# Kernel optimization log

Measured on AMD Instinct MI355X. Metric: run time of the kernel, lower is better.

Reference implementation:

```python
import jax, jax.numpy as jnp
import numpy as np

B, T, H, D = 1, 2048, 32, 128
Q_GROUP = 4
HKV = H // Q_GROUP
INNER = H * D
KV_INNER = HKV * D
ROPE_BASE = 10000.0
NEG = -1e30


def _rope_tables(seq_len, head_dim, dtype):
    inv_freq = 1.0 / (ROPE_BASE ** (jnp.arange(0, head_dim, 2, dtype=jnp.float32) / head_dim))
    t = jnp.arange(seq_len, dtype=jnp.float32)
    freqs = jnp.einsum('t,f->tf', t, inv_freq)          # [T, D/2]
    emb = jnp.concatenate([freqs, freqs], axis=-1)      # [T, D]
    cos = jnp.cos(emb)[None, :, None, :].astype(dtype)  # [1, T, 1, D]
    sin = jnp.sin(emb)[None, :, None, :].astype(dtype)
    return cos, sin


def _rotate(x, cos, sin):
    # x: [B, T, H, D]; split-half rotation: cat(-x2, x1)
    half = x.shape[-1] // 2
    x1, x2 = x[..., :half], x[..., half:]
    x_rot = jnp.concatenate([-x2, x1], axis=-1)
    return x * cos + x_rot * sin


def setup_inputs() -> dict:
    key = jax.random.key(0)
    ks = jax.random.split(key, 5)
    return {
        'stm': jax.random.normal(ks[0], (B, T, H, D), dtype=jnp.float32),
        'w_q': jax.random.normal(ks[1], (INNER, INNER), dtype=jnp.float32) * 0.02,
        'w_k': jax.random.normal(ks[2], (KV_INNER, INNER), dtype=jnp.float32) * 0.02,
        'w_v': jax.random.normal(ks[3], (KV_INNER, INNER), dtype=jnp.float32) * 0.02,
        'w_o': jax.random.normal(ks[4], (INNER, INNER), dtype=jnp.float32) * 0.02,
    }


def reference(stm, w_q, w_k, w_v, w_o):
    b, t, h, d = stm.shape
    x = stm.reshape(b * t, h * d)
    q = x @ w_q.T                                   # [B*T, H*D]
    k = x @ w_k.T                                   # [B*T, Hkv*D]
    v = x @ w_v.T
    # GQA repeat_interleave over query-group axis (broadcast then reshape)
    k = jnp.broadcast_to(k.reshape(b * t, HKV, 1, d), (b * t, HKV, Q_GROUP, d)).reshape(b, t, h, d)
    v = jnp.broadcast_to(v.reshape(b * t, HKV, 1, d), (b * t, HKV, Q_GROUP, d)).reshape(b, t, h, d)
    q = q.reshape(b, t, h, d)
    cos, sin = _rope_tables(t, d, stm.dtype)        # prefill: seq_start = 0
    q = _rotate(q, cos, sin)
    k = _rotate(k, cos, sin)                        # rotated k is what gets written to the KV cache
    scale = 1.0 / np.sqrt(d)
    scores = jnp.einsum('bqhd,bkhd->bhqk', q, k).astype(jnp.float32) * scale
    causal = jnp.tril(jnp.ones((t, t), dtype=jnp.float32))          # mask_w
    bias = (1.0 - causal) * NEG                                     # mask_b
    scores = scores * causal[None, None] + bias[None, None]
    attn = jax.nn.softmax(scores, axis=-1).astype(stm.dtype)
    o = jnp.einsum('bhqk,bkhd->bqhd', attn, v)
    o = o.reshape(b * t, h * d) @ w_o.T
    return o.reshape(b, t, h, d)
```

## Files before the change

### kernel.cpp

```cpp
#include <hip/hip_runtime.h>
#include <hip/hip_bf16.h>
#include <stdint.h>
#include <stddef.h>

using bf16  = __hip_bfloat16;
using v4s   = __attribute__((ext_vector_type(4))) short;
using v8s   = __attribute__((ext_vector_type(8))) short;
using f32x4 = __attribute__((ext_vector_type(4))) float;

#define MFMA_16x16x32(a, b, c) __builtin_amdgcn_mfma_f32_16x16x32_bf16((a), (b), (c), 0, 0, 0)

__device__ __forceinline__ void async_lds16(const bf16* g, bf16* l) {
  __builtin_amdgcn_global_load_lds(
      (const __attribute__((address_space(1))) void*)g,
      (__attribute__((address_space(3))) void*)l, 16, 0, 0);
}

__device__ __forceinline__ short bf16_bits(float f) {
  bf16 h = __float2bfloat16(f);
  short s;
  __builtin_memcpy(&s, &h, sizeof(s));
  return s;
}

__global__ void cvt_f32_bf16(const float* __restrict__ in, bf16* __restrict__ out,
                             int n4) {
  const int i = blockIdx.x * blockDim.x + threadIdx.x;
  if (i >= n4) return;
  const float4 f = ((const float4*)in)[i];
  v4s o;
  o[0] = bf16_bits(f.x);
  o[1] = bf16_bits(f.y);
  o[2] = bf16_bits(f.z);
  o[3] = bf16_bits(f.w);
  *(v4s*)(out + (size_t)i * 4) = o;
}

template <bool F32OUT>
__global__ __launch_bounds__(512, 2) void gemm_bt8(const bf16* __restrict__ A,
                                                   const bf16* __restrict__ B,
                                                   void* __restrict__ C,
                                                   int M, int N, int K) {
  __shared__ bf16 lds[2][64][512];
  const int tid  = threadIdx.x;
  const int w    = tid >> 6;
  const int lane = tid & 63;
  const int quad = lane >> 4;
  const int m16  = lane & 15;
  const int wr = w >> 2, wc = w & 3;
  const int tm = blockIdx.y, tn = blockIdx.x;
  const int NKT = K >> 6;

  const bf16* Ast0 = A + (size_t)(tm * 256 + w * 16 + m16) * K + quad * 8;
  const bf16* Ast1 = Ast0 + (size_t)128 * K;
  const bf16* Bst0 = B + (size_t)(tn * 256 + w * 16 + m16) * K + quad * 8;
  const bf16* Bst1 = Bst0 + (size_t)128 * K;

  auto stage = [&](const bf16* g, bf16* l) {
    async_lds16(g, l);
    async_lds16(g + 32, l + 512);
  };

  f32x4 acc[8][4] = {};

  {
    bf16* L0 = &lds[0][0][0];
    bf16* L1 = &lds[1][0][0];
    stage(Bst0, L0 + (32 + w * 2) * 512);
    stage(Bst1, L0 + (48 + w * 2) * 512);
    stage(Ast0, L0 + (w * 2) * 512);
    stage(Ast1, L0 + (16 + w * 2) * 512);
    stage(Bst0 + 64, L1 + (32 + w * 2) * 512);
    stage(Bst1 + 64, L1 + (48 + w * 2) * 512);
    stage(Ast0 + 64, L1 + (w * 2) * 512);
  }
  asm volatile("s_waitcnt vmcnt(6)" ::: "memory");
  __builtin_amdgcn_s_barrier();

  for (int k = 0; k < NKT; ++k) {
    bf16* Lc = &lds[k & 1][0][0];
    bf16* Ln = &lds[(k & 1) ^ 1][0][0];
    v8s af[4][2], bfv[4][2];
#pragma unroll
    for (int mi = 0; mi < 4; ++mi) {
      af[mi][0] = *(const v8s*)(Lc + ((wr * 8 + mi) * 2 + 0) * 512 + lane * 8);
      af[mi][1] = *(const v8s*)(Lc + ((wr * 8 + mi) * 2 + 1) * 512 + lane * 8);
    }
#pragma unroll
    for (int ni = 0; ni < 4; ++ni) {
      bfv[ni][0] = *(const v8s*)(Lc + (32 + (wc * 4 + ni) * 2 + 0) * 512 + lane * 8);
      bfv[ni][1] = *(const v8s*)(Lc + (32 + (wc * 4 + ni) * 2 + 1) * 512 + lane * 8);
    }
    if (k + 1 < NKT) stage(Ast1 + (size_t)(k + 1) * 64, Ln + (16 + w * 2) * 512);
    __builtin_amdgcn_s_barrier();
    asm volatile("s_waitcnt lgkmcnt(0)" ::: "memory");
    __builtin_amdgcn_sched_barrier(0);
    __builtin_amdgcn_s_setprio(1);
#pragma unroll
    for (int mi = 0; mi < 4; ++mi)
#pragma unroll
      for (int ni = 0; ni < 2; ++ni) {
        acc[mi][ni] = MFMA_16x16x32(af[mi][0], bfv[ni][0], acc[mi][ni]);
        acc[mi][ni] = MFMA_16x16x32(af[mi][1], bfv[ni][1], acc[mi][ni]);
      }
    __builtin_amdgcn_s_setprio(0);
    __builtin_amdgcn_s_barrier();
    if (k + 2 < NKT) stage(Bst0 + (size_t)(k + 2) * 64, Lc + (32 + w * 2) * 512);
    __builtin_amdgcn_s_barrier();
    __builtin_amdgcn_s_setprio(1);
#pragma unroll
    for (int mi = 0; mi < 4; ++mi)
#pragma unroll
      for (int ni = 2; ni < 4; ++ni) {
        acc[mi][ni] = MFMA_16x16x32(af[mi][0], bfv[ni][0], acc[mi][ni]);
        acc[mi][ni] = MFMA_16x16x32(af[mi][1], bfv[ni][1], acc[mi][ni]);
      }
    __builtin_amdgcn_s_setprio(0);
    __builtin_amdgcn_s_barrier();
#pragma unroll
    for (int mi = 0; mi < 4; ++mi) {
      af[mi][0] = *(const v8s*)(Lc + ((wr * 8 + 4 + mi) * 2 + 0) * 512 + lane * 8);
      af[mi][1] = *(const v8s*)(Lc + ((wr * 8 + 4 + mi) * 2 + 1) * 512 + lane * 8);
    }
    if (k + 2 < NKT) stage(Bst1 + (size_t)(k + 2) * 64, Lc + (48 + w * 2) * 512);
    __builtin_amdgcn_s_barrier();
    asm volatile("s_waitcnt lgkmcnt(0)" ::: "memory");
    __builtin_amdgcn_sched_barrier(0);
    __builtin_amdgcn_s_setprio(1);
#pragma unroll
    for (int mi = 0; mi < 4; ++mi)
#pragma unroll
      for (int ni = 0; ni < 2; ++ni) {
        acc[4 + mi][ni] = MFMA_16x16x32(af[mi][0], bfv[ni][0], acc[4 + mi][ni]);
        acc[4 + mi][ni] = MFMA_16x16x32(af[mi][1], bfv[ni][1], acc[4 + mi][ni]);
      }
    __builtin_amdgcn_s_setprio(0);
    __builtin_amdgcn_s_barrier();
    if (k + 2 < NKT) stage(Ast0 + (size_t)(k + 2) * 64, Lc + (w * 2) * 512);
    if (k < NKT - 2) {
      asm volatile("s_waitcnt vmcnt(6)" ::: "memory");
    } else {
      asm volatile("s_waitcnt vmcnt(0)" ::: "memory");
    }
    __builtin_amdgcn_s_barrier();
    __builtin_amdgcn_s_setprio(1);
#pragma unroll
    for (int mi = 0; mi < 4; ++mi)
#pragma unroll
      for (int ni = 2; ni < 4; ++ni) {
        acc[4 + mi][ni] = MFMA_16x16x32(af[mi][0], bfv[ni][0], acc[4 + mi][ni]);
        acc[4 + mi][ni] = MFMA_16x16x32(af[mi][1], bfv[ni][1], acc[4 + mi][ni]);
      }
    __builtin_amdgcn_s_setprio(0);
    __builtin_amdgcn_s_barrier();
  }

#pragma unroll
  for (int mi = 0; mi < 8; ++mi)
#pragma unroll
    for (int ni = 0; ni < 4; ++ni) {
      const int row = tm * 256 + wr * 128 + mi * 16 + quad * 4;
      const int col = tn * 256 + wc * 64 + ni * 16 + m16;
#pragma unroll
      for (int r = 0; r < 4; ++r) {
        if (F32OUT)
          ((float*)C)[(size_t)(row + r) * N + col] = acc[mi][ni][r];
        else
          ((bf16*)C)[(size_t)(row + r) * N + col] = __float2bfloat16(acc[mi][ni][r]);
      }
    }
}

__global__ void rope_kernel(bf16* __restrict__ qkv) {
  const int t  = blockIdx.x;
  const int hh = blockIdx.y;
  const int d  = threadIdx.x;
  const float invf = powf(10000.0f, -(float)(d & 63) * (1.0f / 64.0f));
  const float ang  = (float)t * invf;
  const float c = cosf(ang);
  const float s = sinf(ang);
  const bool isq = (hh < 32);
  bf16* ptr = qkv + (size_t)t * 6144 + (isq ? hh * 128 : 4096 + (hh - 32) * 128);
  const float x   = __bfloat162float(ptr[d]);
  const float xp  = __bfloat162float(ptr[d ^ 64]);
  __syncthreads();
  const float rot = (d < 64) ? -xp : xp;
  const float outv = (x * c + rot * s) * (isq ? 0.08838834764831845f : 1.0f);
  ptr[d] = __float2bfloat16(outv);
}

__global__ void vtrans_kernel(const bf16* __restrict__ qkv, bf16* __restrict__ vt) {
  __shared__ bf16 tile[32][34];
  const int t0 = blockIdx.x * 32, c0 = blockIdx.y * 32;
  const int tx = threadIdx.x, ty = threadIdx.y;
#pragma unroll
  for (int i = 0; i < 4; ++i)
    tile[ty + 8 * i][tx] = qkv[(size_t)(t0 + ty + 8 * i) * 6144 + 5120 + c0 + tx];
  __syncthreads();
#pragma unroll
  for (int i = 0; i < 4; ++i)
    vt[(size_t)(c0 + ty + 8 * i) * 2048 + t0 + tx] = tile[tx][ty + 8 * i];
}

__global__ __launch_bounds__(256) void attn_fused3(const bf16* __restrict__ QKV,
                                                   const bf16* __restrict__ Vt,
                                                   bf16* __restrict__ O) {
  const int qt = 15 - (int)blockIdx.x;
  const int h = blockIdx.y, hk = h >> 2;
  const int tid = threadIdx.x, w = tid >> 6, lane = tid & 63;
  const int quad = lane >> 4, m16 = lane & 15;
  __shared__ bf16 Ks[32 * 512];
  __shared__ bf16 Vs[32 * 512];
  short* Pw = (short*)Ks + w * 4096;

  v8s qf[2][4];
#pragma unroll
  for (int ni = 0; ni < 2; ++ni)
#pragma unroll
    for (int dk = 0; dk < 4; ++dk)
      qf[ni][dk] = *(const v8s*)(QKV + (size_t)(qt * 128 + w * 32 + ni * 16 + m16) * 6144 +
                                 h * 128 + dk * 32 + quad * 8);

  f32x4 acc[8][2] = {};
  float m_run[2] = {-1e30f, -1e30f}, l_run[2] = {0.f, 0.f};

  for (int kt = 0; kt <= qt; ++kt) {
    __syncthreads();
    const bf16* kg = QKV + (size_t)(kt * 128 + m16) * 6144 + 4096 + hk * 128 + w * 32 + quad * 8;
    const bf16* vg = Vt + (size_t)(hk * 128 + m16) * 2048 + kt * 128 + w * 32 + quad * 8;
#pragma unroll
    for (int mi = 0; mi < 8; ++mi) {
      async_lds16(kg + (size_t)mi * 16 * 6144, &Ks[(mi * 4 + w) * 512]);
      async_lds16(vg + (size_t)mi * 16 * 2048, &Vs[(mi * 4 + w) * 512]);
    }
    __syncthreads();
    f32x4 s[8][2];
#pragma unroll
    for (int mi = 0; mi < 8; ++mi) {
      s[mi][0] = f32x4{0.f, 0.f, 0.f, 0.f};
      s[mi][1] = f32x4{0.f, 0.f, 0.f, 0.f};
#pragma unroll
      for (int dk = 0; dk < 4; ++dk) {
        v8s af = *(const v8s*)&Ks[(mi * 4 + dk) * 512 + lane * 8];
        s[mi][0] = MFMA_16x16x32(af, qf[0][dk], s[mi][0]);
        s[mi][1] = MFMA_16x16x32(af, qf[1][dk], s[mi][1]);
      }
    }
    if (kt == qt) {
#pragma unroll
      for (int mi = 0; mi < 8; ++mi)
#pragma unroll
        for (int ni = 0; ni < 2; ++ni)
#pragma unroll
          for (int r = 0; r < 4; ++r)
            if (mi * 16 + quad * 4 + r > w * 32 + ni * 16 + m16) s[mi][ni][r] = -1e30f;
    }
#pragma unroll
    for (int ni = 0; ni < 2; ++ni) {
      float mx = -1e30f;
#pragma unroll
      for (int mi = 0; mi < 8; ++mi)
#pragma unroll
        for (int r = 0; r < 4; ++r) mx = fmaxf(mx, s[mi][ni][r]);
      mx = fmaxf(mx, __shfl_xor(mx, 16));
      mx = fmaxf(mx, __shfl_xor(mx, 32));
      const float mnew = fmaxf(m_run[ni], mx);
      const float alpha = __expf(m_run[ni] - mnew);
      m_run[ni] = mnew;
      float rs = 0.f;
#pragma unroll
      for (int mi = 0; mi < 8; ++mi)
#pragma unroll
        for (int r = 0; r < 4; ++r) {
          const float p = __expf(s[mi][ni][r] - mnew);
          s[mi][ni][r] = p;
          rs += p;
        }
      rs += __shfl_xor(rs, 16);
      rs += __shfl_xor(rs, 32);
      l_run[ni] = l_run[ni] * alpha + rs;
#pragma unroll
      for (int mi2 = 0; mi2 < 8; ++mi2)
#pragma unroll
        for (int r = 0; r < 4; ++r) acc[mi2][ni][r] *= alpha;
    }
    __syncthreads();
#pragma unroll
    for (int mi = 0; mi < 8; ++mi)
#pragma unroll
      for (int ni = 0; ni < 2; ++ni) {
        v4s p4;
#pragma unroll
        for (int r = 0; r < 4; ++r) p4[r] = bf16_bits(s[mi][ni][r]);
        const int base = (ni * 4 + (mi >> 1)) * 512 +
                         ((mi & 1) * 2 + (quad >> 1)) * 128 + m16 * 8 + (quad & 1) * 4;
        *(v4s*)&Pw[base] = p4;
      }
    asm volatile("" ::: "memory");
#pragma unroll
    for (int kp = 0; kp < 4; ++kp) {
      v8s pf0 = *(const v8s*)&Pw[(0 * 4 + kp) * 512 + lane * 8];
      v8s pf1 = *(const v8s*)&Pw[(1 * 4 + kp) * 512 + lane * 8];
#pragma unroll
      for (int mi2 = 0; mi2 < 8; ++mi2) {
        v8s vf = *(const v8s*)&Vs[(mi2 * 4 + kp) * 512 + lane * 8];
        acc[mi2][0] = MFMA_16x16x32(vf, pf0, acc[mi2][0]);
        acc[mi2][1] = MFMA_16x16x32(vf, pf1, acc[mi2][1]);
      }
    }
  }
#pragma unroll
  for (int ni = 0; ni < 2; ++ni) {
    const float rl = 1.0f / l_run[ni];
    const size_t qrow = qt * 128 + w * 32 + ni * 16 + m16;
#pragma unroll
    for (int mi2 = 0; mi2 < 8; ++mi2) {
      v4s o4;
#pragma unroll
      for (int r = 0; r < 4; ++r) o4[r] = bf16_bits(acc[mi2][ni][r] * rl);
      *(v4s*)(O + qrow * 4096 + h * 128 + mi2 * 16 + quad * 4) = o4;
    }
  }
}

extern "C" void kernel_launch(void* const* d_in, const int* in_sizes, int n_in,
                              void* d_out, int out_size, void* d_ws, size_t ws_size,
                              hipStream_t stream) {
  const float* stm = (const float*)d_in[0];
  const float* w_q = (const float*)d_in[1];
  const float* w_k = (const float*)d_in[2];
  const float* w_v = (const float*)d_in[3];
  const float* w_o = (const float*)d_in[4];
  float* out = (float*)d_out;

  const size_t M_STM = (size_t)2048 * 4096;
  const size_t M_WQ  = (size_t)4096 * 4096;
  const size_t M_WK  = (size_t)1024 * 4096;

  bf16* ws      = (bf16*)d_ws;
  bf16* wqkv_bf = ws;
  bf16* wo_bf   = ws;
  bf16* vT      = ws + M_WQ;
  bf16* stm_bf  = ws + 24 * 1024 * 1024;
  bf16* o_buf   = stm_bf;
  bf16* qkv_buf = ws + 32 * 1024 * 1024;

  cvt_f32_bf16<<<(int)(M_STM / 1024), 256, 0, stream>>>(stm, stm_bf, (int)(M_STM / 4));
  cvt_f32_bf16<<<(int)(M_WQ / 1024), 256, 0, stream>>>(w_q, wqkv_bf, (int)(M_WQ / 4));
  cvt_f32_bf16<<<(int)(M_WK / 1024), 256, 0, stream>>>(w_k, wqkv_bf + M_WQ, (int)(M_WK / 4));
  cvt_f32_bf16<<<(int)(M_WK / 1024), 256, 0, stream>>>(w_v, wqkv_bf + M_WQ + M_WK, (int)(M_WK / 4));

  gemm_bt8<false><<<dim3(24, 8), 512, 0, stream>>>(stm_bf, wqkv_bf, qkv_buf, 2048, 6144, 4096);

  cvt_f32_bf16<<<(int)(M_WQ / 1024), 256, 0, stream>>>(w_o, wo_bf, (int)(M_WQ / 4));

  rope_kernel<<<dim3(2048, 40), 128, 0, stream>>>(qkv_buf);
  vtrans_kernel<<<dim3(64, 32), dim3(32, 8), 0, stream>>>(qkv_buf, vT);
  attn_fused3<<<dim3(16, 32), 256, 0, stream>>>(qkv_buf, vT, o_buf);

  gemm_bt8<true><<<dim3(16, 8), 512, 0, stream>>>(o_buf, wo_bf, out, 2048, 4096, 4096);
}
```

Measured before the change: 680.1 us.

## Pipeline K/V tile prefetch in attention with separate P buffer and split PV

Restructures the attention loop so the next K tile is prefetched asynchronously right after QK^T, and the next V tile after PV. This overlaps global-to-LDS loads with compute instead of blocking at the top of every iteration. P moves to its own LDS buffer and is written and consumed in two halves, with MFMA priority raised around the matrix phases. Half the heads now walk query tiles in reverse order, to balance causal work across the grid. The cost is extra LDS, which may reduce occupancy, and hand-written waitcnt/barrier sequencing that is fragile.

```diff
diff --git a/kernel.cpp b/kernel.cpp
--- a/kernel.cpp
+++ b/kernel.cpp
@@ -202,16 +202,19 @@
     vt[(size_t)(c0 + ty + 8 * i) * 2048 + t0 + tx] = tile[tx][ty + 8 * i];
 }
 
-__global__ __launch_bounds__(256) void attn_fused3(const bf16* __restrict__ QKV,
+__global__ __launch_bounds__(256) void attn_fused4(const bf16* __restrict__ QKV,
                                                    const bf16* __restrict__ Vt,
                                                    bf16* __restrict__ O) {
-  const int qt = 15 - (int)blockIdx.x;
-  const int h = blockIdx.y, hk = h >> 2;
+  const int bx = (int)blockIdx.x;
+  const int h  = (int)blockIdx.y;
+  const int qt = (h < 16) ? (15 - bx) : bx;
+  const int hk = h >> 2;
   const int tid = threadIdx.x, w = tid >> 6, lane = tid & 63;
   const int quad = lane >> 4, m16 = lane & 15;
   __shared__ bf16 Ks[32 * 512];
   __shared__ bf16 Vs[32 * 512];
-  short* Pw = (short*)Ks + w * 4096;
+  __shared__ __attribute__((aligned(16))) short Ps[4][2048];
+  short* Pw = Ps[w];
 
   v8s qf[2][4];
 #pragma unroll
@@ -221,20 +224,24 @@
       qf[ni][dk] = *(const v8s*)(QKV + (size_t)(qt * 128 + w * 32 + ni * 16 + m16) * 6144 +
                                  h * 128 + dk * 32 + quad * 8);
 
+  const bf16* kg = QKV + (size_t)m16 * 6144 + 4096 + hk * 128 + w * 32 + quad * 8;
+  const bf16* vg = Vt + (size_t)(hk * 128 + m16) * 2048 + w * 32 + quad * 8;
+
   f32x4 acc[8][2] = {};
   float m_run[2] = {-1e30f, -1e30f}, l_run[2] = {0.f, 0.f};
 
+#pragma unroll
+  for (int mi = 0; mi < 8; ++mi)
+    async_lds16(kg + (size_t)mi * 16 * 6144, &Ks[(mi * 4 + w) * 512]);
+#pragma unroll
+  for (int mi = 0; mi < 8; ++mi)
+    async_lds16(vg + (size_t)mi * 16 * 2048, &Vs[(mi * 4 + w) * 512]);
+
   for (int kt = 0; kt <= qt; ++kt) {
-    __syncthreads();
-    const bf16* kg = QKV + (size_t)(kt * 128 + m16) * 6144 + 4096 + hk * 128 + w * 32 + quad * 8;
-    const bf16* vg = Vt + (size_t)(hk * 128 + m16) * 2048 + kt * 128 + w * 32 + quad * 8;
-#pragma unroll
-    for (int mi = 0; mi < 8; ++mi) {
-      async_lds16(kg + (size_t)mi * 16 * 6144, &Ks[(mi * 4 + w) * 512]);
-      async_lds16(vg + (size_t)mi * 16 * 2048, &Vs[(mi * 4 + w) * 512]);
-    }
-    __syncthreads();
+    asm volatile("s_waitcnt vmcnt(8)" ::: "memory");
+    __builtin_amdgcn_s_barrier();
     f32x4 s[8][2];
+    __builtin_amdgcn_s_setprio(1);
 #pragma unroll
     for (int mi = 0; mi < 8; ++mi) {
       s[mi][0] = f32x4{0.f, 0.f, 0.f, 0.f};
@@ -245,6 +252,15 @@
         s[mi][0] = MFMA_16x16x32(af, qf[0][dk], s[mi][0]);
         s[mi][1] = MFMA_16x16x32(af, qf[1][dk], s[mi][1]);
       }
+    }
+    __builtin_amdgcn_s_setprio(0);
+    asm volatile("s_waitcnt vmcnt(0)" ::: "memory");
+    __builtin_amdgcn_s_barrier();
+    if (kt < qt) {
+      const bf16* kg2 = kg + (size_t)(kt + 1) * 128 * 6144;
+#pragma unroll
+      for (int mi = 0; mi < 8; ++mi)
+        async_lds16(kg2 + (size_t)mi * 16 * 6144, &Ks[(mi * 4 + w) * 512]);
     }
     if (kt == qt) {
 #pragma unroll
@@ -284,29 +300,65 @@
 #pragma unroll
         for (int r = 0; r < 4; ++r) acc[mi2][ni][r] *= alpha;
     }
-    __syncthreads();
-#pragma unroll
-    for (int mi = 0; mi < 8; ++mi)
+#pragma unroll
+    for (int mi = 0; mi < 4; ++mi)
 #pragma unroll
       for (int ni = 0; ni < 2; ++ni) {
         v4s p4;
 #pragma unroll
         for (int r = 0; r < 4; ++r) p4[r] = bf16_bits(s[mi][ni][r]);
-        const int base = (ni * 4 + (mi >> 1)) * 512 +
+        const int base = (ni * 2 + (mi >> 1)) * 512 +
                          ((mi & 1) * 2 + (quad >> 1)) * 128 + m16 * 8 + (quad & 1) * 4;
         *(v4s*)&Pw[base] = p4;
       }
     asm volatile("" ::: "memory");
-#pragma unroll
-    for (int kp = 0; kp < 4; ++kp) {
-      v8s pf0 = *(const v8s*)&Pw[(0 * 4 + kp) * 512 + lane * 8];
-      v8s pf1 = *(const v8s*)&Pw[(1 * 4 + kp) * 512 + lane * 8];
+    __builtin_amdgcn_s_setprio(1);
+#pragma unroll
+    for (int kpl = 0; kpl < 2; ++kpl) {
+      v8s pf0 = *(const v8s*)&Pw[(0 * 2 + kpl) * 512 + lane * 8];
+      v8s pf1 = *(const v8s*)&Pw[(1 * 2 + kpl) * 512 + lane * 8];
 #pragma unroll
       for (int mi2 = 0; mi2 < 8; ++mi2) {
-        v8s vf = *(const v8s*)&Vs[(mi2 * 4 + kp) * 512 + lane * 8];
+        v8s vf = *(const v8s*)&Vs[(mi2 * 4 + kpl) * 512 + lane * 8];
         acc[mi2][0] = MFMA_16x16x32(vf, pf0, acc[mi2][0]);
         acc[mi2][1] = MFMA_16x16x32(vf, pf1, acc[mi2][1]);
       }
+    }
+    __builtin_amdgcn_s_setprio(0);
+    asm volatile("" ::: "memory");
+#pragma unroll
+    for (int mi = 4; mi < 8; ++mi)
+#pragma unroll
+      for (int ni = 0; ni < 2; ++ni) {
+        const int mloc = mi - 4;
+        v4s p4;
+#pragma unroll
+        for (int r = 0; r < 4; ++r) p4[r] = bf16_bits(s[mi][ni][r]);
+        const int base = (ni * 2 + (mloc >> 1)) * 512 +
+                         ((mloc & 1) * 2 + (quad >> 1)) * 128 + m16 * 8 + (quad & 1) * 4;
+        *(v4s*)&Pw[base] = p4;
+      }
+    asm volatile("" ::: "memory");
+    __builtin_amdgcn_s_setprio(1);
+#pragma unroll
+    for (int kpl = 0; kpl < 2; ++kpl) {
+      v8s pf0 = *(const v8s*)&Pw[(0 * 2 + kpl) * 512 + lane * 8];
+      v8s pf1 = *(const v8s*)&Pw[(1 * 2 + kpl) * 512 + lane * 8];
+#pragma unroll
+      for (int mi2 = 0; mi2 < 8; ++mi2) {
+        v8s vf = *(const v8s*)&Vs[(mi2 * 4 + 2 + kpl) * 512 + lane * 8];
+        acc[mi2][0] = MFMA_16x16x32(vf, pf0, acc[mi2][0]);
+        acc[mi2][1] = MFMA_16x16x32(vf, pf1, acc[mi2][1]);
+      }
+    }
+    __builtin_amdgcn_s_setprio(0);
+    asm volatile("" ::: "memory");
+    __builtin_amdgcn_s_barrier();
+    if (kt < qt) {
+      const bf16* vg2 = vg + (size_t)(kt + 1) * 128;
+#pragma unroll
+      for (int mi = 0; mi < 8; ++mi)
+        async_lds16(vg2 + (size_t)mi * 16 * 2048, &Vs[(mi * 4 + w) * 512]);
     }
   }
 #pragma unroll
@@ -356,7 +408,7 @@
 
   rope_kernel<<<dim3(2048, 40), 128, 0, stream>>>(qkv_buf);
   vtrans_kernel<<<dim3(64, 32), dim3(32, 8), 0, stream>>>(qkv_buf, vT);
-  attn_fused3<<<dim3(16, 32), 256, 0, stream>>>(qkv_buf, vT, o_buf);
+  attn_fused4<<<dim3(16, 32), 256, 0, stream>>>(qkv_buf, vT, o_buf);
 
   gemm_bt8<true><<<dim3(16, 8), 512, 0, stream>>>(o_buf, wo_bf, out, 2048, 4096, 4096);
 }
```

After: 627.8 us. -7.7%, faster.
